# Kernel tuning notes

Hardware: AMD Instinct MI355X
Metric: run time of the kernel (lower is better)

The kernel has to match this reference:

```python
import jax, jax.numpy as jnp
import numpy as np

N_NODES = 50000
N_EDGES = 800000
D = 128        # input_dim == output_dim
D_EDGE = 64    # edge_attr_size
Z_DIM = 2 * D + D_EDGE  # 320


def setup_inputs() -> dict:
    key = jax.random.key(0)
    k1, k2, k3, k4, k5 = jax.random.split(key, 5)
    x = jax.random.normal(k1, (N_NODES, D), dtype=jnp.float32)
    edge_index = jax.random.randint(k2, (2, N_EDGES), 0, N_NODES, dtype=jnp.int64)
    edge_attr = jax.random.normal(k3, (N_EDGES, D_EDGE), dtype=jnp.float32)
    scale = 1.0 / np.sqrt(Z_DIM)
    W_f = jax.random.normal(k4, (Z_DIM, D), dtype=jnp.float32) * scale
    W_s = jax.random.normal(k5, (Z_DIM, D), dtype=jnp.float32) * scale
    b_f = jnp.zeros((D,), dtype=jnp.float32)
    b_s = jnp.zeros((D,), dtype=jnp.float32)
    return {"x": x, "edge_index": edge_index, "edge_attr": edge_attr,
            "W_f": W_f, "b_f": b_f, "W_s": W_s, "b_s": b_s}


def reference(x, edge_index, edge_attr, W_f, b_f, W_s, b_s):
    # Dropout(p=0.0) is identity in inference.
    src = edge_index[0]  # j (message source)
    dst = edge_index[1]  # i (message target)
    # z_e = [x_i, x_j, e_ij]  -> [E, 2D + D_edge]
    z = jnp.concatenate([x[dst], x[src], edge_attr], axis=-1)
    # CGConv message: sigmoid(lin_f(z)) * softplus(lin_s(z))
    msg = jax.nn.sigmoid(z @ W_f + b_f) * jax.nn.softplus(z @ W_s + b_s)
    # scatter-add aggregation + residual
    out = jax.ops.segment_sum(msg, dst, num_segments=x.shape[0]) + x
    # use_activation=True -> ReLU
    return jax.nn.relu(out)
```

## Files before the change

kernel.cpp:

```cpp
#include <hip/hip_runtime.h>
#include <hip/hip_bf16.h>

#define E_TOTAL   800000
#define NN        50000
#define DD        128
#define DE        64
#define ZDIM      320
#define MT        64

typedef short bf16x8 __attribute__((ext_vector_type(8)));
typedef float f32x4  __attribute__((ext_vector_type(4)));

__device__ __forceinline__ unsigned short f2bf(float f) {
    union { float f; unsigned int u; } v; v.f = f;
    unsigned int u = v.u;
    return (unsigned short)((u + 0x7fffu + ((u >> 16) & 1u)) >> 16);
}

__device__ __forceinline__ unsigned pkbf2(float a, float b) {
    __hip_bfloat162 h = __float22bfloat162_rn(make_float2(a, b));
    unsigned u; __builtin_memcpy(&u, &h, 4); return u;
}

__device__ __forceinline__ uint2 pkbf4(float4 v) {
    uint2 r; r.x = pkbf2(v.x, v.y); r.y = pkbf2(v.z, v.w); return r;
}

__device__ __forceinline__ float fast_rcp(float x) {
#if __has_builtin(__builtin_amdgcn_rcpf)
    return __builtin_amdgcn_rcpf(x);
#else
    return 1.0f / x;
#endif
}

__global__ void prep_kernel(const float* __restrict__ x,
                            const float* __restrict__ W_f,
                            const float* __restrict__ W_s,
                            unsigned short* __restrict__ Wt,
                            float* __restrict__ out) {
    int id = blockIdx.x * 256 + threadIdx.x;
    if (id < NN * DD / 4)
        ((float4*)out)[id] = ((const float4*)x)[id];
    if (id < 2 * DD * ZDIM) {
        int n = id / ZDIM, k = id - n * ZDIM;
        float wv = (n < DD) ? W_f[k * DD + n] : W_s[k * DD + (n - DD)];
        Wt[n * ZDIM + k] = f2bf(wv);
    }
}

__global__ __launch_bounds__(256, 3)
void edge_kernel(const float* __restrict__ x,
                 const int* __restrict__ ei,
                 const float* __restrict__ ea,
                 const unsigned short* __restrict__ Wt,
                 const float* __restrict__ bf_,
                 const float* __restrict__ bs_,
                 float* __restrict__ out) {
    __shared__ unsigned short A_lds[MT * ZDIM];
    __shared__ int dst_lds[MT];
    __shared__ int src_lds[MT];

    const int t = threadIdx.x;
    const int m_off = blockIdx.x * MT;
    const int lane = t & 63;
    const int w = t >> 6;
    const int l15 = lane & 15;
    const int quad = lane >> 4;

    if (t < MT) dst_lds[t] = ei[E_TOTAL + m_off + t];
    else if (t < 2 * MT) src_lds[t - MT] = ei[m_off + (t - MT)];
    __syncthreads();

    #pragma unroll
    for (int it = 0; it < 4; ++it) {
        int idx = it * 256 + t;
        int e = idx >> 4, kq = idx & 15;
        float4 v = ((const float4*)(ea + (size_t)(m_off + e) * DE))[kq];
        int g = 32 + (kq >> 1);
        int col = ((g & ~7) | ((g & 7) ^ (e & 7))) * 8 + (kq & 1) * 4;
        *((uint2*)&A_lds[e * ZDIM + col]) = pkbf4(v);
    }
    #pragma unroll
    for (int it = 0; it < 8; ++it) {
        int idx = it * 256 + t;
        int e = idx >> 5, kq = idx & 31;
        float4 v = ((const float4*)(x + (size_t)dst_lds[e] * DD))[kq];
        int g = kq >> 1;
        int col = ((g & ~7) | ((g & 7) ^ (e & 7))) * 8 + (kq & 1) * 4;
        *((uint2*)&A_lds[e * ZDIM + col]) = pkbf4(v);
    }
    #pragma unroll
    for (int it = 0; it < 8; ++it) {
        int idx = it * 256 + t;
        int e = idx >> 5, kq = idx & 31;
        float4 v = ((const float4*)(x + (size_t)src_lds[e] * DD))[kq];
        int g = 16 + (kq >> 1);
        int col = ((g & ~7) | ((g & 7) ^ (e & 7))) * 8 + (kq & 1) * 4;
        *((uint2*)&A_lds[e * ZDIM + col]) = pkbf4(v);
    }

    f32x4 acc[4][4] = {};
    const int nt0 = 2 * w;

    const unsigned short* Bp[4];
    #pragma unroll
    for (int u = 0; u < 4; ++u) {
        int nt = nt0 + ((u < 2) ? u : (6 + u));
        Bp[u] = Wt + (size_t)(nt * 16 + l15) * ZDIM + quad * 8;
    }

    __syncthreads();

    #pragma unroll
    for (int kc = 0; kc < 5; ++kc) {
        #pragma unroll
        for (int ks = 0; ks < 2; ++ks) {
            bf16x8 af[4], bfr[4];
            #pragma unroll
            for (int i = 0; i < 4; ++i) {
                int m = i * 16 + l15;
                int g = 8 * kc + 4 * ks + quad;
                int col = ((g & ~7) | ((g & 7) ^ (l15 & 7))) * 8;
                af[i] = *((const bf16x8*)&A_lds[m * ZDIM + col]);
            }
            #pragma unroll
            for (int u = 0; u < 4; ++u)
                bfr[u] = *((const bf16x8*)(Bp[u] + kc * 64 + ks * 32));
            #pragma unroll
            for (int i = 0; i < 4; ++i)
                #pragma unroll
                for (int u = 0; u < 4; ++u)
                    acc[i][u] = __builtin_amdgcn_mfma_f32_16x16x32_bf16(
                        af[i], bfr[u], acc[i][u], 0, 0, 0);
        }
    }

    const int c0 = 32 * w + l15;
    const int c1 = c0 + 16;
    const float bf0 = bf_[c0], bs0 = bs_[c0];
    const float bf1 = bf_[c1], bs1 = bs_[c1];

    #pragma unroll
    for (int i = 0; i < 4; ++i) {
        #pragma unroll
        for (int j = 0; j < 4; ++j) {
            int e = i * 16 + quad * 4 + j;
            float* op = out + (size_t)dst_lds[e] * DD;
            float f0 = acc[i][0][j] + bf0;
            float s0 = acc[i][2][j] + bs0;
            float m0 = fast_rcp(1.0f + __expf(-f0)) *
                       (fmaxf(s0, 0.0f) + __logf(1.0f + __expf(-fabsf(s0))));
            atomicAdd(op + c0, m0);
            float f1 = acc[i][1][j] + bf1;
            float s1 = acc[i][3][j] + bs1;
            float m1 = fast_rcp(1.0f + __expf(-f1)) *
                       (fmaxf(s1, 0.0f) + __logf(1.0f + __expf(-fabsf(s1))));
            atomicAdd(op + c1, m1);
        }
    }
}

__global__ void relu_kernel(float* __restrict__ out) {
    int id = blockIdx.x * 256 + threadIdx.x;
    if (id < NN * DD / 4) {
        float4 v = ((float4*)out)[id];
        v.x = fmaxf(v.x, 0.0f); v.y = fmaxf(v.y, 0.0f);
        v.z = fmaxf(v.z, 0.0f); v.w = fmaxf(v.w, 0.0f);
        ((float4*)out)[id] = v;
    }
}

extern "C" void kernel_launch(void* const* d_in, const int* in_sizes, int n_in,
                              void* d_out, int out_size, void* d_ws, size_t ws_size,
                              hipStream_t stream) {
    (void)in_sizes; (void)n_in; (void)out_size; (void)ws_size;
    const float* x   = (const float*)d_in[0];
    const int*   ei  = (const int*)d_in[1];
    const float* ea  = (const float*)d_in[2];
    const float* W_f = (const float*)d_in[3];
    const float* b_f = (const float*)d_in[4];
    const float* W_s = (const float*)d_in[5];
    const float* b_s = (const float*)d_in[6];
    float* out = (float*)d_out;
    unsigned short* Wt = (unsigned short*)d_ws;

    prep_kernel<<<6250, 256, 0, stream>>>(x, W_f, W_s, Wt, out);
    edge_kernel<<<E_TOTAL / MT, 256, 0, stream>>>(x, ei, ea, Wt, b_f, b_s, out);
    relu_kernel<<<6250, 256, 0, stream>>>(out);
}
```

Before: 665.0 us.

## Sort edges by destination and pre-reduce messages before atomic scatter

Adds a counting sort of edges by destination (histogram, single-block scan, scatter) and runs the edge kernel on the sorted order. Lanes then add up consecutive messages to the same destination in registers and issue one atomic per run instead of one per edge. With ~16 edges per node and 64-edge tiles, runs are often long enough to cut atomic traffic. In exchange it adds four extra launches, a serial one-block scan, and random-order reads of edge_attr through the permutation. The path only runs when the workspace is large enough.

```diff
diff --git a/kernel.cpp b/kernel.cpp
--- a/kernel.cpp
+++ b/kernel.cpp
@@ -49,6 +49,48 @@
     }
 }
 
+__global__ void hist_kernel(const int* __restrict__ ei, int* __restrict__ counts) {
+    int e = blockIdx.x * 256 + threadIdx.x;
+    if (e < E_TOTAL) atomicAdd(&counts[ei[E_TOTAL + e]], 1);
+}
+
+__global__ __launch_bounds__(1024)
+void scan_kernel(const int* __restrict__ counts, int* __restrict__ cursor) {
+    __shared__ int part[1024];
+    int t = threadIdx.x;
+    const int PER = 49;
+    int base = t * PER;
+    int s = 0;
+    for (int i = 0; i < PER; ++i) { int k = base + i; s += (k < NN) ? counts[k] : 0; }
+    part[t] = s;
+    __syncthreads();
+    for (int d = 1; d < 1024; d <<= 1) {
+        int v = (t >= d) ? part[t - d] : 0;
+        __syncthreads();
+        part[t] += v;
+        __syncthreads();
+    }
+    int run = (t == 0) ? 0 : part[t - 1];
+    for (int i = 0; i < PER; ++i) {
+        int k = base + i;
+        if (k < NN) { cursor[k] = run; run += counts[k]; }
+    }
+}
+
+__global__ void scatter_kernel(const int* __restrict__ ei, int* __restrict__ cursor,
+                               int* __restrict__ sdst, int* __restrict__ ssrc,
+                               int* __restrict__ seid) {
+    int e = blockIdx.x * 256 + threadIdx.x;
+    if (e < E_TOTAL) {
+        int d = ei[E_TOTAL + e];
+        int pos = atomicAdd(&cursor[d], 1);
+        sdst[pos] = d;
+        ssrc[pos] = ei[e];
+        seid[pos] = e;
+    }
+}
+
+template<bool SORTED>
 __global__ __launch_bounds__(256, 3)
 void edge_kernel(const float* __restrict__ x,
                  const int* __restrict__ ei,
@@ -56,10 +98,14 @@
                  const unsigned short* __restrict__ Wt,
                  const float* __restrict__ bf_,
                  const float* __restrict__ bs_,
-                 float* __restrict__ out) {
+                 float* __restrict__ out,
+                 const int* __restrict__ sdst,
+                 const int* __restrict__ ssrc,
+                 const int* __restrict__ seid) {
     __shared__ unsigned short A_lds[MT * ZDIM];
     __shared__ int dst_lds[MT];
     __shared__ int src_lds[MT];
+    __shared__ int eid_lds[MT];
 
     const int t = threadIdx.x;
     const int m_off = blockIdx.x * MT;
@@ -68,15 +114,22 @@
     const int l15 = lane & 15;
     const int quad = lane >> 4;
 
-    if (t < MT) dst_lds[t] = ei[E_TOTAL + m_off + t];
-    else if (t < 2 * MT) src_lds[t - MT] = ei[m_off + (t - MT)];
+    if (SORTED) {
+        if (t < MT) dst_lds[t] = sdst[m_off + t];
+        else if (t < 2 * MT) src_lds[t - MT] = ssrc[m_off + t - MT];
+        else if (t < 3 * MT) eid_lds[t - 2 * MT] = seid[m_off + t - 2 * MT];
+    } else {
+        if (t < MT) dst_lds[t] = ei[E_TOTAL + m_off + t];
+        else if (t < 2 * MT) src_lds[t - MT] = ei[m_off + (t - MT)];
+    }
     __syncthreads();
 
     #pragma unroll
     for (int it = 0; it < 4; ++it) {
         int idx = it * 256 + t;
         int e = idx >> 4, kq = idx & 15;
-        float4 v = ((const float4*)(ea + (size_t)(m_off + e) * DE))[kq];
+        int row = SORTED ? eid_lds[e] : (m_off + e);
+        float4 v = ((const float4*)(ea + (size_t)row * DE))[kq];
         int g = 32 + (kq >> 1);
         int col = ((g & ~7) | ((g & 7) ^ (e & 7))) * 8 + (kq & 1) * 4;
         *((uint2*)&A_lds[e * ZDIM + col]) = pkbf4(v);
@@ -141,22 +194,49 @@
     const float bf0 = bf_[c0], bs0 = bs_[c0];
     const float bf1 = bf_[c1], bs1 = bs_[c1];
 
-    #pragma unroll
-    for (int i = 0; i < 4; ++i) {
+    if (SORTED) {
+        int d = -1; float s0 = 0.0f, s1 = 0.0f;
         #pragma unroll
-        for (int j = 0; j < 4; ++j) {
-            int e = i * 16 + quad * 4 + j;
-            float* op = out + (size_t)dst_lds[e] * DD;
-            float f0 = acc[i][0][j] + bf0;
-            float s0 = acc[i][2][j] + bs0;
-            float m0 = fast_rcp(1.0f + __expf(-f0)) *
-                       (fmaxf(s0, 0.0f) + __logf(1.0f + __expf(-fabsf(s0))));
-            atomicAdd(op + c0, m0);
-            float f1 = acc[i][1][j] + bf1;
-            float s1 = acc[i][3][j] + bs1;
-            float m1 = fast_rcp(1.0f + __expf(-f1)) *
-                       (fmaxf(s1, 0.0f) + __logf(1.0f + __expf(-fabsf(s1))));
-            atomicAdd(op + c1, m1);
+        for (int i = 0; i < 4; ++i) {
+            #pragma unroll
+            for (int j = 0; j < 4; ++j) {
+                int e = i * 16 + quad * 4 + j;
+                int dd = dst_lds[e];
+                if (dd != d) {
+                    if (d >= 0) {
+                        atomicAdd(out + (size_t)d * DD + c0, s0);
+                        atomicAdd(out + (size_t)d * DD + c1, s1);
+                    }
+                    d = dd; s0 = 0.0f; s1 = 0.0f;
+                }
+                float f0 = acc[i][0][j] + bf0;
+                float sg0 = acc[i][2][j] + bs0;
+                s0 += fast_rcp(1.0f + __expf(-f0)) *
+                      (fmaxf(sg0, 0.0f) + __logf(1.0f + __expf(-fabsf(sg0))));
+                float f1 = acc[i][1][j] + bf1;
+                float sg1 = acc[i][3][j] + bs1;
+                s1 += fast_rcp(1.0f + __expf(-f1)) *
+                      (fmaxf(sg1, 0.0f) + __logf(1.0f + __expf(-fabsf(sg1))));
+            }
+        }
+        atomicAdd(out + (size_t)d * DD + c0, s0);
+        atomicAdd(out + (size_t)d * DD + c1, s1);
+    } else {
+        #pragma unroll
+        for (int i = 0; i < 4; ++i) {
+            #pragma unroll
+            for (int j = 0; j < 4; ++j) {
+                int e = i * 16 + quad * 4 + j;
+                float* op = out + (size_t)dst_lds[e] * DD;
+                float f0 = acc[i][0][j] + bf0;
+                float sg0 = acc[i][2][j] + bs0;
+                atomicAdd(op + c0, fast_rcp(1.0f + __expf(-f0)) *
+                    (fmaxf(sg0, 0.0f) + __logf(1.0f + __expf(-fabsf(sg0)))));
+                float f1 = acc[i][1][j] + bf1;
+                float sg1 = acc[i][3][j] + bs1;
+                atomicAdd(op + c1, fast_rcp(1.0f + __expf(-f1)) *
+                    (fmaxf(sg1, 0.0f) + __logf(1.0f + __expf(-fabsf(sg1)))));
+            }
         }
     }
 }
@@ -174,7 +254,7 @@
 extern "C" void kernel_launch(void* const* d_in, const int* in_sizes, int n_in,
                               void* d_out, int out_size, void* d_ws, size_t ws_size,
                               hipStream_t stream) {
-    (void)in_sizes; (void)n_in; (void)out_size; (void)ws_size;
+    (void)in_sizes; (void)n_in; (void)out_size;
     const float* x   = (const float*)d_in[0];
     const int*   ei  = (const int*)d_in[1];
     const float* ea  = (const float*)d_in[2];
@@ -183,9 +263,29 @@
     const float* W_s = (const float*)d_in[5];
     const float* b_s = (const float*)d_in[6];
     float* out = (float*)d_out;
-    unsigned short* Wt = (unsigned short*)d_ws;
+
+    char* ws = (char*)d_ws;
+    unsigned short* Wt = (unsigned short*)ws;
+    int* counts = (int*)(ws + 163840);
+    int* cursor = (int*)(ws + 363840);
+    int* sdst   = (int*)(ws + 563840);
+    int* ssrc   = (int*)(ws + 3763840);
+    int* seid   = (int*)(ws + 6963840);
+    const size_t WS_NEED = 10163840;
 
     prep_kernel<<<6250, 256, 0, stream>>>(x, W_f, W_s, Wt, out);
-    edge_kernel<<<E_TOTAL / MT, 256, 0, stream>>>(x, ei, ea, Wt, b_f, b_s, out);
+
+    if (ws_size >= WS_NEED) {
+        hipMemsetAsync(counts, 0, NN * sizeof(int), stream);
+        hist_kernel<<<3125, 256, 0, stream>>>(ei, counts);
+        scan_kernel<<<1, 1024, 0, stream>>>(counts, cursor);
+        scatter_kernel<<<3125, 256, 0, stream>>>(ei, cursor, sdst, ssrc, seid);
+        edge_kernel<true><<<E_TOTAL / MT, 256, 0, stream>>>(
+            x, ei, ea, Wt, b_f, b_s, out, sdst, ssrc, seid);
+    } else {
+        edge_kernel<false><<<E_TOTAL / MT, 256, 0, stream>>>(
+            x, ei, ea, Wt, b_f, b_s, out, nullptr, nullptr, nullptr);
+    }
+
     relu_kernel<<<6250, 256, 0, stream>>>(out);
 }
```

New measurement: 814.2 us. 1.22x slower.

## Precompute per-node dst projection and sort edges by destination to merge atomics

Applied to the files above, without the earlier changes.

Splits the 320-wide GEMM so the x_dst part (128 of K) runs once per node in a node kernel, with bias folded in and the result stored as bf16. The edge GEMM then covers only K=192. Edges are counting-sorted by destination (count, scan, scatter), so each lane can accumulate runs of equal dst in registers before issuing an atomic. This adds several small preprocessing kernels, a gathered edge_attr access through the permutation, and extra bf16 rounding of the node projection. The src and dst indices are packed into 16 bits each, which breaks for ids of 65536 or more.

```diff
diff --git a/kernel.cpp b/kernel.cpp
--- a/kernel.cpp
+++ b/kernel.cpp
@@ -6,7 +6,9 @@
 #define DD        128
 #define DE        64
 #define ZDIM      320
+#define KE        192
 #define MT        64
+#define NBS       196
 
 typedef short bf16x8 __attribute__((ext_vector_type(8)));
 typedef float f32x4  __attribute__((ext_vector_type(4)));
@@ -15,6 +17,10 @@
     union { float f; unsigned int u; } v; v.f = f;
     unsigned int u = v.u;
     return (unsigned short)((u + 0x7fffu + ((u >> 16) & 1u)) >> 16);
+}
+
+__device__ __forceinline__ float bf2f(unsigned short h) {
+    union { unsigned u; float f; } v; v.u = ((unsigned)h) << 16; return v.f;
 }
 
 __device__ __forceinline__ unsigned pkbf2(float a, float b) {
@@ -34,11 +40,279 @@
 #endif
 }
 
+
 __global__ void prep_kernel(const float* __restrict__ x,
+                            const int* __restrict__ ei,
                             const float* __restrict__ W_f,
                             const float* __restrict__ W_s,
-                            unsigned short* __restrict__ Wt,
+                            unsigned short* __restrict__ WtE,
+                            unsigned short* __restrict__ WtN,
+                            int* __restrict__ counts,
                             float* __restrict__ out) {
+    int id = blockIdx.x * 256 + threadIdx.x;
+    ((float4*)out)[id] = ((const float4*)x)[id];
+    if (id < E_TOTAL) atomicAdd(&counts[ei[E_TOTAL + id]], 1);
+    if (id < 256 * KE) {
+        int n = id / KE, k = id - n * KE;
+        int ok = 128 + k;
+        float wv = (n < DD) ? W_f[ok * DD + n] : W_s[ok * DD + (n - DD)];
+        WtE[id] = f2bf(wv);
+    } else if (id < 256 * KE + 256 * DD) {
+        int id2 = id - 256 * KE;
+        int n = id2 / DD, k = id2 - n * DD;
+        float wv = (n < DD) ? W_f[k * DD + n] : W_s[k * DD + (n - DD)];
+        WtN[id2] = f2bf(wv);
+    }
+}
+
+__global__ void scan_part(const int* __restrict__ counts, int* __restrict__ partial) {
+    __shared__ int red[256];
+    int t = threadIdx.x, k = blockIdx.x * 256 + t;
+    red[t] = (k < NN) ? counts[k] : 0;
+    __syncthreads();
+    for (int d = 128; d > 0; d >>= 1) {
+        if (t < d) red[t] += red[t + d];
+        __syncthreads();
+    }
+    if (t == 0) partial[blockIdx.x] = red[0];
+}
+
+__global__ void scan_top(int* __restrict__ partial) {
+    __shared__ int s[256];
+    int t = threadIdx.x;
+    int v = (t < NBS) ? partial[t] : 0;
+    s[t] = v; __syncthreads();
+    for (int d = 1; d < 256; d <<= 1) {
+        int a = (t >= d) ? s[t - d] : 0;
+        __syncthreads();
+        s[t] += a;
+        __syncthreads();
+    }
+    if (t < NBS) partial[t] = s[t] - v;
+}
+
+__global__ void scan_final(const int* __restrict__ counts,
+                           const int* __restrict__ partial,
+                           int* __restrict__ cursor) {
+    __shared__ int s[256];
+    int t = threadIdx.x, k = blockIdx.x * 256 + t;
+    int v = (k < NN) ? counts[k] : 0;
+    s[t] = v; __syncthreads();
+    for (int d = 1; d < 256; d <<= 1) {
+        int a = (t >= d) ? s[t - d] : 0;
+        __syncthreads();
+        s[t] += a;
+        __syncthreads();
+    }
+    if (k < NN) cursor[k] = partial[blockIdx.x] + s[t] - v;
+}
+
+__global__ void scatter_kernel(const int* __restrict__ ei, int* __restrict__ cursor,
+                               unsigned* __restrict__ spak, int* __restrict__ seid) {
+    int e = blockIdx.x * 256 + threadIdx.x;
+    if (e < E_TOTAL) {
+        int d = ei[E_TOTAL + e];
+        int pos = atomicAdd(&cursor[d], 1);
+        spak[pos] = ((unsigned)d << 16) | (unsigned)ei[e];
+        seid[pos] = e;
+    }
+}
+
+__global__ __launch_bounds__(256, 4)
+void node_kernel(const float* __restrict__ x,
+                 const unsigned short* __restrict__ WtN,
+                 const float* __restrict__ bf_, const float* __restrict__ bs_,
+                 unsigned short* __restrict__ nodeFS) {
+    __shared__ unsigned short A_lds[MT * DD];
+    const int t = threadIdx.x;
+    const int m_off = blockIdx.x * MT;
+    const int lane = t & 63, w = t >> 6, l15 = lane & 15, quad = lane >> 4;
+
+    #pragma unroll
+    for (int it = 0; it < 8; ++it) {
+        int idx = it * 256 + t;
+        int e = idx >> 5, kq = idx & 31;
+        int row = m_off + e; if (row >= NN) row = NN - 1;
+        float4 v = ((const float4*)(x + (size_t)row * DD))[kq];
+        int g = kq >> 1;
+        int col = ((g & ~7) | ((g & 7) ^ (e & 7))) * 8 + (kq & 1) * 4;
+        *((uint2*)&A_lds[e * DD + col]) = pkbf4(v);
+    }
+
+    f32x4 acc[4][4] = {};
+    const int nt0 = 2 * w;
+    const unsigned short* Bp[4];
+    #pragma unroll
+    for (int u = 0; u < 4; ++u) {
+        int nt = nt0 + ((u < 2) ? u : (6 + u));
+        Bp[u] = WtN + (size_t)(nt * 16 + l15) * DD + quad * 8;
+    }
+    __syncthreads();
+
+    #pragma unroll
+    for (int ks = 0; ks < 4; ++ks) {
+        bf16x8 af[4], bfr[4];
+        #pragma unroll
+        for (int i = 0; i < 4; ++i) {
+            int m = i * 16 + l15;
+            int g = 4 * ks + quad;
+            int col = ((g & ~7) | ((g & 7) ^ (l15 & 7))) * 8;
+            af[i] = *((const bf16x8*)&A_lds[m * DD + col]);
+        }
+        #pragma unroll
+        for (int u = 0; u < 4; ++u)
+            bfr[u] = *((const bf16x8*)(Bp[u] + ks * 32));
+        #pragma unroll
+        for (int i = 0; i < 4; ++i)
+            #pragma unroll
+            for (int u = 0; u < 4; ++u)
+                acc[i][u] = __builtin_amdgcn_mfma_f32_16x16x32_bf16(
+                    af[i], bfr[u], acc[i][u], 0, 0, 0);
+    }
+
+    const int c0 = 32 * w + l15, c1 = c0 + 16;
+    const float bf0 = bf_[c0], bs0 = bs_[c0], bf1 = bf_[c1], bs1 = bs_[c1];
+    #pragma unroll
+    for (int i = 0; i < 4; ++i)
+        #pragma unroll
+        for (int j = 0; j < 4; ++j) {
+            int e = i * 16 + quad * 4 + j;
+            int row = m_off + e;
+            if (row < NN) {
+                unsigned short* p = nodeFS + (size_t)row * 256;
+                p[c0]       = f2bf(acc[i][0][j] + bf0);
+                p[c1]       = f2bf(acc[i][1][j] + bf1);
+                p[128 + c0] = f2bf(acc[i][2][j] + bs0);
+                p[128 + c1] = f2bf(acc[i][3][j] + bs1);
+            }
+        }
+}
+
+__global__ __launch_bounds__(256, 6)
+void edge_kernel(const float* __restrict__ x,
+                 const float* __restrict__ ea,
+                 const unsigned short* __restrict__ WtE,
+                 const unsigned short* __restrict__ nodeFS,
+                 float* __restrict__ out,
+                 const unsigned* __restrict__ spak,
+                 const int* __restrict__ seid) {
+    __shared__ unsigned short A_lds[MT * KE];
+    __shared__ int dst_lds[MT];
+    __shared__ int src_lds[MT];
+    __shared__ int eid_lds[MT];
+
+    const int t = threadIdx.x;
+    const int m_off = blockIdx.x * MT;
+    const int lane = t & 63, w = t >> 6, l15 = lane & 15, quad = lane >> 4;
+
+    if (t < MT) {
+        unsigned p = spak[m_off + t];
+        dst_lds[t] = (int)(p >> 16);
+        src_lds[t] = (int)(p & 0xffffu);
+    } else if (t < 2 * MT) {
+        eid_lds[t - MT] = seid[m_off + t - MT];
+    }
+    __syncthreads();
+
+    #pragma unroll
+    for (int it = 0; it < 4; ++it) {
+        int idx = it * 256 + t;
+        int e = idx >> 4, kq = idx & 15;
+        float4 v = ((const float4*)(ea + (size_t)eid_lds[e] * DE))[kq];
+        int g = 16 + (kq >> 1);
+        int col = ((g & ~7) | ((g & 7) ^ (e & 7))) * 8 + (kq & 1) * 4;
+        *((uint2*)&A_lds[e * KE + col]) = pkbf4(v);
+    }
+    #pragma unroll
+    for (int it = 0; it < 8; ++it) {
+        int idx = it * 256 + t;
+        int e = idx >> 5, kq = idx & 31;
+        float4 v = ((const float4*)(x + (size_t)src_lds[e] * DD))[kq];
+        int g = kq >> 1;
+        int col = ((g & ~7) | ((g & 7) ^ (e & 7))) * 8 + (kq & 1) * 4;
+        *((uint2*)&A_lds[e * KE + col]) = pkbf4(v);
+    }
+
+    f32x4 acc[4][4] = {};
+    const int nt0 = 2 * w;
+    const unsigned short* Bp[4];
+    #pragma unroll
+    for (int u = 0; u < 4; ++u) {
+        int nt = nt0 + ((u < 2) ? u : (6 + u));
+        Bp[u] = WtE + (size_t)(nt * 16 + l15) * KE + quad * 8;
+    }
+    __syncthreads();
+
+    #pragma unroll
+    for (int ks = 0; ks < 6; ++ks) {
+        bf16x8 af[4], bfr[4];
+        #pragma unroll
+        for (int i = 0; i < 4; ++i) {
+            int m = i * 16 + l15;
+            int g = 4 * ks + quad;
+            int col = ((g & ~7) | ((g & 7) ^ (l15 & 7))) * 8;
+            af[i] = *((const bf16x8*)&A_lds[m * KE + col]);
+        }
+        #pragma unroll
+        for (int u = 0; u < 4; ++u)
+            bfr[u] = *((const bf16x8*)(Bp[u] + ks * 32));
+        #pragma unroll
+        for (int i = 0; i < 4; ++i)
+            #pragma unroll
+            for (int u = 0; u < 4; ++u)
+                acc[i][u] = __builtin_amdgcn_mfma_f32_16x16x32_bf16(
+                    af[i], bfr[u], acc[i][u], 0, 0, 0);
+    }
+
+    const int c0 = 32 * w + l15, c1 = c0 + 16;
+
+    int d = -1;
+    float s0 = 0.f, s1 = 0.f, nf0 = 0.f, ns0 = 0.f, nf1 = 0.f, ns1 = 0.f;
+    #pragma unroll
+    for (int i = 0; i < 4; ++i)
+        #pragma unroll
+        for (int j = 0; j < 4; ++j) {
+            int e = i * 16 + quad * 4 + j;
+            int dd = dst_lds[e];
+            if (dd != d) {
+                if (d >= 0) {
+                    atomicAdd(out + (size_t)d * DD + c0, s0);
+                    atomicAdd(out + (size_t)d * DD + c1, s1);
+                }
+                d = dd; s0 = 0.f; s1 = 0.f;
+                const unsigned short* p = nodeFS + (size_t)d * 256;
+                nf0 = bf2f(p[c0]);       nf1 = bf2f(p[c1]);
+                ns0 = bf2f(p[128 + c0]); ns1 = bf2f(p[128 + c1]);
+            }
+            float f0  = acc[i][0][j] + nf0;
+            float sg0 = acc[i][2][j] + ns0;
+            s0 += fast_rcp(1.f + __expf(-f0)) *
+                  (fmaxf(sg0, 0.f) + __logf(1.f + __expf(-fabsf(sg0))));
+            float f1  = acc[i][1][j] + nf1;
+            float sg1 = acc[i][3][j] + ns1;
+            s1 += fast_rcp(1.f + __expf(-f1)) *
+                  (fmaxf(sg1, 0.f) + __logf(1.f + __expf(-fabsf(sg1))));
+        }
+    atomicAdd(out + (size_t)d * DD + c0, s0);
+    atomicAdd(out + (size_t)d * DD + c1, s1);
+}
+
+__global__ void relu_kernel(float* __restrict__ out) {
+    int id = blockIdx.x * 256 + threadIdx.x;
+    if (id < NN * DD / 4) {
+        float4 v = ((float4*)out)[id];
+        v.x = fmaxf(v.x, 0.0f); v.y = fmaxf(v.y, 0.0f);
+        v.z = fmaxf(v.z, 0.0f); v.w = fmaxf(v.w, 0.0f);
+        ((float4*)out)[id] = v;
+    }
+}
+
+
+__global__ void prep_fb(const float* __restrict__ x,
+                        const float* __restrict__ W_f,
+                        const float* __restrict__ W_s,
+                        unsigned short* __restrict__ Wt,
+                        float* __restrict__ out) {
     int id = blockIdx.x * 256 + threadIdx.x;
     if (id < NN * DD / 4)
         ((float4*)out)[id] = ((const float4*)x)[id];
@@ -50,23 +324,20 @@
 }
 
 __global__ __launch_bounds__(256, 3)
-void edge_kernel(const float* __restrict__ x,
-                 const int* __restrict__ ei,
-                 const float* __restrict__ ea,
-                 const unsigned short* __restrict__ Wt,
-                 const float* __restrict__ bf_,
-                 const float* __restrict__ bs_,
-                 float* __restrict__ out) {
+void edge_fb(const float* __restrict__ x,
+             const int* __restrict__ ei,
+             const float* __restrict__ ea,
+             const unsigned short* __restrict__ Wt,
+             const float* __restrict__ bf_,
+             const float* __restrict__ bs_,
+             float* __restrict__ out) {
     __shared__ unsigned short A_lds[MT * ZDIM];
     __shared__ int dst_lds[MT];
     __shared__ int src_lds[MT];
 
     const int t = threadIdx.x;
     const int m_off = blockIdx.x * MT;
-    const int lane = t & 63;
-    const int w = t >> 6;
-    const int l15 = lane & 15;
-    const int quad = lane >> 4;
+    const int lane = t & 63, w = t >> 6, l15 = lane & 15, quad = lane >> 4;
 
     if (t < MT) dst_lds[t] = ei[E_TOTAL + m_off + t];
     else if (t < 2 * MT) src_lds[t - MT] = ei[m_off + (t - MT)];
@@ -102,79 +373,59 @@
 
     f32x4 acc[4][4] = {};
     const int nt0 = 2 * w;
-
     const unsigned short* Bp[4];
     #pragma unroll
     for (int u = 0; u < 4; ++u) {
         int nt = nt0 + ((u < 2) ? u : (6 + u));
         Bp[u] = Wt + (size_t)(nt * 16 + l15) * ZDIM + quad * 8;
     }
-
-    __syncthreads();
-
-    #pragma unroll
-    for (int kc = 0; kc < 5; ++kc) {
-        #pragma unroll
-        for (int ks = 0; ks < 2; ++ks) {
-            bf16x8 af[4], bfr[4];
-            #pragma unroll
-            for (int i = 0; i < 4; ++i) {
-                int m = i * 16 + l15;
-                int g = 8 * kc + 4 * ks + quad;
-                int col = ((g & ~7) | ((g & 7) ^ (l15 & 7))) * 8;
-                af[i] = *((const bf16x8*)&A_lds[m * ZDIM + col]);
-            }
+    __syncthreads();
+
+    #pragma unroll
+    for (int ks = 0; ks < 10; ++ks) {
+        bf16x8 af[4], bfr[4];
+        #pragma unroll
+        for (int i = 0; i < 4; ++i) {
+            int m = i * 16 + l15;
+            int g = 4 * ks + quad;
+            int col = ((g & ~7) | ((g & 7) ^ (l15 & 7))) * 8;
+            af[i] = *((const bf16x8*)&A_lds[m * ZDIM + col]);
+        }
+        #pragma unroll
+        for (int u = 0; u < 4; ++u)
+            bfr[u] = *((const bf16x8*)(Bp[u] + ks * 32));
+        #pragma unroll
+        for (int i = 0; i < 4; ++i)
             #pragma unroll
             for (int u = 0; u < 4; ++u)
-                bfr[u] = *((const bf16x8*)(Bp[u] + kc * 64 + ks * 32));
-            #pragma unroll
-            for (int i = 0; i < 4; ++i)
-                #pragma unroll
-                for (int u = 0; u < 4; ++u)
-                    acc[i][u] = __builtin_amdgcn_mfma_f32_16x16x32_bf16(
-                        af[i], bfr[u], acc[i][u], 0, 0, 0);
-        }
-    }
-
-    const int c0 = 32 * w + l15;
-    const int c1 = c0 + 16;
-    const float bf0 = bf_[c0], bs0 = bs_[c0];
-    const float bf1 = bf_[c1], bs1 = bs_[c1];
-
-    #pragma unroll
-    for (int i = 0; i < 4; ++i) {
+                acc[i][u] = __builtin_amdgcn_mfma_f32_16x16x32_bf16(
+                    af[i], bfr[u], acc[i][u], 0, 0, 0);
+    }
+
+    const int c0 = 32 * w + l15, c1 = c0 + 16;
+    const float bf0 = bf_[c0], bs0 = bs_[c0], bf1 = bf_[c1], bs1 = bs_[c1];
+    #pragma unroll
+    for (int i = 0; i < 4; ++i)
         #pragma unroll
         for (int j = 0; j < 4; ++j) {
             int e = i * 16 + quad * 4 + j;
             float* op = out + (size_t)dst_lds[e] * DD;
             float f0 = acc[i][0][j] + bf0;
-            float s0 = acc[i][2][j] + bs0;
-            float m0 = fast_rcp(1.0f + __expf(-f0)) *
-                       (fmaxf(s0, 0.0f) + __logf(1.0f + __expf(-fabsf(s0))));
-            atomicAdd(op + c0, m0);
+            float sg0 = acc[i][2][j] + bs0;
+            atomicAdd(op + c0, fast_rcp(1.f + __expf(-f0)) *
+                (fmaxf(sg0, 0.f) + __logf(1.f + __expf(-fabsf(sg0)))));
             float f1 = acc[i][1][j] + bf1;
-            float s1 = acc[i][3][j] + bs1;
-            float m1 = fast_rcp(1.0f + __expf(-f1)) *
-                       (fmaxf(s1, 0.0f) + __logf(1.0f + __expf(-fabsf(s1))));
-            atomicAdd(op + c1, m1);
-        }
-    }
-}
-
-__global__ void relu_kernel(float* __restrict__ out) {
-    int id = blockIdx.x * 256 + threadIdx.x;
-    if (id < NN * DD / 4) {
-        float4 v = ((float4*)out)[id];
-        v.x = fmaxf(v.x, 0.0f); v.y = fmaxf(v.y, 0.0f);
-        v.z = fmaxf(v.z, 0.0f); v.w = fmaxf(v.w, 0.0f);
-        ((float4*)out)[id] = v;
-    }
-}
+            float sg1 = acc[i][3][j] + bs1;
+            atomicAdd(op + c1, fast_rcp(1.f + __expf(-f1)) *
+                (fmaxf(sg1, 0.f) + __logf(1.f + __expf(-fabsf(sg1)))));
+        }
+}
+
 
 extern "C" void kernel_launch(void* const* d_in, const int* in_sizes, int n_in,
                               void* d_out, int out_size, void* d_ws, size_t ws_size,
                               hipStream_t stream) {
-    (void)in_sizes; (void)n_in; (void)out_size; (void)ws_size;
+    (void)in_sizes; (void)n_in; (void)out_size;
     const float* x   = (const float*)d_in[0];
     const int*   ei  = (const int*)d_in[1];
     const float* ea  = (const float*)d_in[2];
@@ -183,9 +434,34 @@
     const float* W_s = (const float*)d_in[5];
     const float* b_s = (const float*)d_in[6];
     float* out = (float*)d_out;
-    unsigned short* Wt = (unsigned short*)d_ws;
-
-    prep_kernel<<<6250, 256, 0, stream>>>(x, W_f, W_s, Wt, out);
-    edge_kernel<<<E_TOTAL / MT, 256, 0, stream>>>(x, ei, ea, Wt, b_f, b_s, out);
+
+    char* ws = (char*)d_ws;
+    unsigned short* WtE    = (unsigned short*)ws;
+    unsigned short* WtN    = (unsigned short*)(ws + 98304);
+    int*            counts = (int*)(ws + 163840);
+    int*            cursor = (int*)(ws + 363840);
+    int*            partial= (int*)(ws + 563840);
+    unsigned*       spak   = (unsigned*)(ws + 564864);
+    int*            seid   = (int*)(ws + 3764864);
+    unsigned short* nodeFS = (unsigned short*)(ws + 6964864);
+    const size_t WS_NEED = 32564864;
+
+    if (ws_size >= WS_NEED) {
+        hipMemsetAsync(counts, 0, NN * sizeof(int), stream);
+        prep_kernel<<<NN * DD / 4 / 256, 256, 0, stream>>>(
+            x, ei, W_f, W_s, WtE, WtN, counts, out);
+        scan_part<<<NBS, 256, 0, stream>>>(counts, partial);
+        scan_top<<<1, 256, 0, stream>>>(partial);
+        scan_final<<<NBS, 256, 0, stream>>>(counts, partial, cursor);
+        scatter_kernel<<<(E_TOTAL + 255) / 256, 256, 0, stream>>>(ei, cursor, spak, seid);
+        node_kernel<<<(NN + MT - 1) / MT, 256, 0, stream>>>(x, WtN, b_f, b_s, nodeFS);
+        edge_kernel<<<E_TOTAL / MT, 256, 0, stream>>>(
+            x, ea, WtE, nodeFS, out, spak, seid);
+    } else {
+        unsigned short* Wt = (unsigned short*)ws;
+        prep_fb<<<6250, 256, 0, stream>>>(x, W_f, W_s, Wt, out);
+        edge_fb<<<E_TOTAL / MT, 256, 0, stream>>>(x, ei, ea, Wt, b_f, b_s, out);
+    }
+
     relu_kernel<<<6250, 256, 0, stream>>>(out);
 }
```

New measurement: 1.245 ms. 1.87x slower.
